# Kernel tuning notes

Hardware: AMD Instinct MI355X
Metric: run time of the kernel (lower is better)

Reference implementation:

```python
import jax, jax.numpy as jnp
import numpy as np
from jax import lax

WS = 7          # window_size
SHIFT = 0       # shift_size
HEADS = 6
EPS = 1e-12     # torch F.normalize default eps


def _window_partition(x, ws):
    B, C, H, W = x.shape
    x = x.reshape(B, C, H // ws, ws, W // ws, ws)
    # (B, H/ws, W/ws, C, ws, ws) -> (B*nW, C, ws, ws)
    return x.transpose(0, 2, 4, 1, 3, 5).reshape(-1, C, ws, ws)


def _window_reverse(win, B, C, H, W, ws):
    x = win.reshape(B, H // ws, W // ws, C, ws, ws)
    return x.transpose(0, 3, 1, 4, 2, 5).reshape(B, C, H, W)


def setup_inputs() -> dict:
    key = jax.random.key(0)
    ks = jax.random.split(key, 7)
    C = 192
    inp = {
        "x": jax.random.normal(ks[0], (4, C, 224, 224), jnp.float32),
        "w_qkv": jax.random.normal(ks[1], (3 * C, C), jnp.float32) * 0.02,
        "b_qkv": jax.random.normal(ks[2], (3 * C,), jnp.float32) * 0.02,
        "w_dw": jax.random.normal(ks[3], (3 * C, 1, 3, 3), jnp.float32) * 0.02,
        "b_dw": jax.random.normal(ks[4], (3 * C,), jnp.float32) * 0.02,
        "w_proj": jax.random.normal(ks[5], (C, C), jnp.float32) * 0.02,
        "b_proj": jax.random.normal(ks[6], (C,), jnp.float32) * 0.02,
        "temperature": jnp.ones((HEADS, 1, 1), jnp.float32),
    }
    return inp


def reference(x, w_qkv, b_qkv, w_dw, b_dw, w_proj, b_proj, temperature):
    B, C, H, W = x.shape
    pad_h = (WS - H % WS) % WS
    pad_w = (WS - W % WS) % WS
    if pad_h or pad_w:
        x = jnp.pad(x, ((0, 0), (0, 0), (0, pad_h), (0, pad_w)))
    Hp, Wp = H + pad_h, W + pad_w
    if SHIFT > 0:
        x = jnp.roll(x, shift=(-SHIFT, -SHIFT), axis=(2, 3))

    xw = _window_partition(x, WS)                     # (nW, C, ws, ws)

    # 1x1 conv qkv
    qkv = jnp.einsum('bchw,oc->bohw', xw, w_qkv) + b_qkv[None, :, None, None]
    # depthwise 3x3 conv, padding=1, groups=3C
    qkv = lax.conv_general_dilated(
        qkv, w_dw, window_strides=(1, 1), padding=((1, 1), (1, 1)),
        feature_group_count=3 * C,
        dimension_numbers=('NCHW', 'OIHW', 'NCHW')) + b_dw[None, :, None, None]

    q, k, v = jnp.split(qkv, 3, axis=1)               # each (nW, C, ws, ws)
    nW = q.shape[0]
    c = C // HEADS
    hw = WS * WS

    def heads(t):
        return t.reshape(nW, HEADS, c, hw)            # (nW, h, c, hw)

    q, k, v = heads(q), heads(k), heads(v)
    q = q / jnp.maximum(jnp.linalg.norm(q, axis=-2, keepdims=True), EPS)
    k = k / jnp.maximum(jnp.linalg.norm(k, axis=-2, keepdims=True), EPS)

    # attn[b,h,n,m] = sum_c k[b,h,c,n] * q[b,h,c,m], scaled by per-head temperature
    attn = jnp.einsum('bhcn,bhcm->bhnm', k, q) * temperature[None]
    attn = jax.nn.softmax(attn, axis=-2)
    out = jnp.einsum('bhcn,bhnm->bhcm', v, attn)      # (nW, h, c, hw)

    out = out.reshape(nW, C, WS, WS)
    out = _window_reverse(out, B, C, Hp, Wp, WS)
    out = jnp.einsum('bchw,oc->bohw', out, w_proj) + b_proj[None, :, None, None]

    if SHIFT > 0:
        out = jnp.roll(out, shift=(SHIFT, SHIFT), axis=(2, 3))
    if pad_h or pad_w:
        out = out[:, :, :H, :W]
    return out
```

## Files before the change

### kernel.cpp

```cpp
#include <hip/hip_runtime.h>
#include <math.h>

namespace {
constexpr int WSZ   = 7;
constexpr int HW    = 49;
constexpr int CIN   = 192;
constexpr int HEADS = 6;
constexpr int CH    = 32;
constexpr int IMG   = 224;
constexpr int ASTR  = 54;

__global__ __launch_bounds__(512, 4)
void win_attn_fused(const float* __restrict__ x,
                    const float* __restrict__ w_qkv,
                    const float* __restrict__ b_qkv,
                    const float* __restrict__ w_dw,
                    const float* __restrict__ b_dw,
                    const float* __restrict__ w_proj,
                    const float* __restrict__ b_proj,
                    const float* __restrict__ temperature,
                    float* __restrict__ out)
{
    __shared__ float xs[CIN][HW];
    __shared__ float qh[96][HW];
    __shared__ float attnb[HW][ASTR];
    __shared__ float outb[CH][HW];

    const int tid  = threadIdx.x;
    const int lane = tid & 63;
    const int wv   = __builtin_amdgcn_readfirstlane(tid >> 6);

    const int wi   = blockIdx.x;
    const int b    = wi >> 10;
    const int hy   = (wi >> 5) & 31;
    const int wx   = wi & 31;
    const int row0 = hy * WSZ, col0 = wx * WSZ;

    const int  p   = lane;
    const bool act = (lane < HW);
    const int  py  = p / WSZ, px = p % WSZ;

    for (int i = tid; i < CIN * HW; i += 512) {
        int c = i / HW, pp = i - c * HW;
        int gy = row0 + pp / WSZ, gx = col0 + pp % WSZ;
        xs[c][pp] = x[((b * CIN + c) * IMG + gy) * IMG + gx];
    }
    __syncthreads();

    float pacc[24];
    #pragma unroll
    for (int j = 0; j < 24; ++j) pacc[j] = 0.f;

    for (int h = 0; h < HEADS; ++h) {
        int oj[12];
        #pragma unroll
        for (int j = 0; j < 12; ++j) {
            int r = 12 * wv + j;
            oj[j] = (r < 32) ? (CH * h + r)
                  : (r < 64) ? (CIN + CH * h + (r - 32))
                             : (2 * CIN + CH * h + (r - 64));
        }

        if (act) {
            float acc[12];
            #pragma unroll
            for (int j = 0; j < 12; ++j) acc[j] = 0.f;
            #pragma unroll 4
            for (int c = 0; c < CIN; ++c) {
                float xv = xs[c][p];
                #pragma unroll
                for (int j = 0; j < 12; ++j)
                    acc[j] = fmaf(w_qkv[oj[j] * CIN + c], xv, acc[j]);
            }
            #pragma unroll
            for (int j = 0; j < 12; ++j)
                qh[12 * wv + j][p] = acc[j] + b_qkv[oj[j]];
        }

        if (act) {
            float cv[12];
            #pragma unroll
            for (int j = 0; j < 12; ++j) {
                int r = 12 * wv + j, o = oj[j];
                float s = b_dw[o];
                #pragma unroll
                for (int ky = 0; ky < 3; ++ky) {
                    int yy = py + ky - 1;
                    #pragma unroll
                    for (int kx = 0; kx < 3; ++kx) {
                        int xx = px + kx - 1;
                        bool ok = (yy >= 0) & (yy < WSZ) & (xx >= 0) & (xx < WSZ);
                        float v = ok ? qh[r][yy * WSZ + xx] : 0.f;
                        s = fmaf(w_dw[o * 9 + ky * 3 + kx], v, s);
                    }
                }
                cv[j] = s;
            }
            #pragma unroll
            for (int j = 0; j < 12; ++j) qh[12 * wv + j][p] = cv[j];
        }
        __syncthreads();

        float rnq = 0.f, rnk = 0.f;
        if (act) {
            float sq = 0.f, sk = 0.f;
            #pragma unroll
            for (int cc = 0; cc < CH; ++cc) {
                float a  = qh[cc][p];      sq = fmaf(a, a, sq);
                float bb = qh[CH + cc][p]; sk = fmaf(bb, bb, sk);
            }
            rnq = 1.0f / fmaxf(sqrtf(sq), 1e-12f);
            rnk = 1.0f / fmaxf(sqrtf(sk), 1e-12f);
        }

        float qreg[CH];
        if (act) {
            #pragma unroll
            for (int cc = 0; cc < CH; ++cc) qreg[cc] = qh[cc][p];
        }

        const float tmp = temperature[h];
        {
            int n0 = (wv * HW) >> 3;
            int n1 = ((wv + 1) * HW) >> 3;
            for (int n = n0; n < n1; ++n) {
                float rkn = __shfl(rnk, n);
                if (act) {
                    float s = 0.f;
                    #pragma unroll
                    for (int cc = 0; cc < CH; ++cc)
                        s = fmaf(qh[CH + cc][n], qreg[cc], s);
                    attnb[n][p] = s * tmp * rkn * rnq;
                }
            }
        }
        __syncthreads();

        {
            int m = tid >> 3, sub = tid & 7;
            if (m < HW) {
                int na = (sub * HW) >> 3;
                int nb = ((sub + 1) * HW) >> 3;
                float mx = -1e30f;
                for (int n = na; n < nb; ++n) mx = fmaxf(mx, attnb[n][m]);
                mx = fmaxf(mx, __shfl_xor(mx, 1));
                mx = fmaxf(mx, __shfl_xor(mx, 2));
                mx = fmaxf(mx, __shfl_xor(mx, 4));
                float sum = 0.f;
                for (int n = na; n < nb; ++n) {
                    float e = __expf(attnb[n][m] - mx);
                    attnb[n][m] = e;
                    sum += e;
                }
                sum += __shfl_xor(sum, 1);
                sum += __shfl_xor(sum, 2);
                sum += __shfl_xor(sum, 4);
                float inv = 1.0f / sum;
                for (int n = na; n < nb; ++n) attnb[n][m] *= inv;
            }
        }
        __syncthreads();

        if (act) {
            float s[4];
            #pragma unroll
            for (int j = 0; j < 4; ++j) s[j] = 0.f;
            for (int n = 0; n < HW; ++n) {
                float a = attnb[n][p];
                #pragma unroll
                for (int j = 0; j < 4; ++j)
                    s[j] = fmaf(qh[2 * CH + 4 * wv + j][n], a, s[j]);
            }
            #pragma unroll
            for (int j = 0; j < 4; ++j) outb[4 * wv + j][p] = s[j];
        }
        __syncthreads();

        if (act) {
            #pragma unroll 4
            for (int cc = 0; cc < CH; ++cc) {
                float ov = outb[cc][p];
                #pragma unroll
                for (int j = 0; j < 24; ++j)
                    pacc[j] = fmaf(w_proj[(24 * wv + j) * CIN + CH * h + cc], ov, pacc[j]);
            }
        }
    }

    if (act) {
        #pragma unroll
        for (int j = 0; j < 24; ++j) {
            int oc = 24 * wv + j;
            out[((b * CIN + oc) * IMG + row0 + py) * IMG + col0 + px] = pacc[j] + b_proj[oc];
        }
    }
}
}

extern "C" void kernel_launch(void* const* d_in, const int* in_sizes, int n_in,
                              void* d_out, int out_size, void* d_ws, size_t ws_size,
                              hipStream_t stream) {
    const float* x      = (const float*)d_in[0];
    const float* w_qkv  = (const float*)d_in[1];
    const float* b_qkv  = (const float*)d_in[2];
    const float* w_dw   = (const float*)d_in[3];
    const float* b_dw   = (const float*)d_in[4];
    const float* w_proj = (const float*)d_in[5];
    const float* b_proj = (const float*)d_in[6];
    const float* temp   = (const float*)d_in[7];

    win_attn_fused<<<dim3(4096), dim3(512), 0, stream>>>(
        x, w_qkv, b_qkv, w_dw, b_dw, w_proj, b_proj, temp, (float*)d_out);
}
```

Measured before the change: 4.515 ms.

## Stage windows through workspace with pre/post transpose kernels and float4 LDS reads

Adds a pre-pass kernel that copies image rows through shared memory into a contiguous per-window layout in the workspace, and a post-pass that scatters window outputs back to NCHW. The main kernel now reads each window as one contiguous chunk and stores it in LDS transposed (pixel-major, padded stride) so the QKV projection can use float4 LDS loads. The aim is to replace the strided 7-element global reads and writes of the fused kernel with coalesced traffic, at the price of an extra round trip of the full tensor through global memory and two more launches. A fallback to the original direct kernel runs when the workspace is too small.

```diff
diff --git a/kernel.cpp b/kernel.cpp
--- a/kernel.cpp
+++ b/kernel.cpp
@@ -9,19 +9,64 @@
 constexpr int CH    = 32;
 constexpr int IMG   = 224;
 constexpr int ASTR  = 54;
+constexpr int XSTR  = 196;
+constexpr int NWX   = 32;
+constexpr int CHUNK = CIN * HW;
+constexpr int NWIN  = 4 * 32 * 32;
+
+__global__ void win_pre(const float* __restrict__ x, float* __restrict__ win)
+{
+    __shared__ float tile[8][WSZ][IMG];
+    const int blk = blockIdx.x;
+    const int cg  = blk % 24;
+    const int hy  = (blk / 24) % 32;
+    const int b   = blk / (24 * 32);
+    const int c0  = cg * 8, row0 = hy * WSZ;
+
+    for (int i = threadIdx.x; i < 8 * WSZ * IMG; i += 256) {
+        int gx = i % IMG, ry = (i / IMG) % WSZ, c = i / (IMG * WSZ);
+        tile[c][ry][gx] = x[(((size_t)(b * CIN + c0 + c)) * IMG + row0 + ry) * IMG + gx];
+    }
+    __syncthreads();
+    for (int i = threadIdx.x; i < NWX * 8 * HW; i += 256) {
+        int p = i % HW, c = (i / HW) % 8, wx = i / (HW * 8);
+        size_t wi = ((size_t)(b * 32 + hy)) * NWX + wx;
+        win[wi * CHUNK + (c0 + c) * HW + p] = tile[c][p / WSZ][wx * WSZ + p % WSZ];
+    }
+}
+
+__global__ void win_post(const float* __restrict__ win, float* __restrict__ out)
+{
+    __shared__ float tile[8][WSZ][IMG];
+    const int blk = blockIdx.x;
+    const int cg  = blk % 24;
+    const int hy  = (blk / 24) % 32;
+    const int b   = blk / (24 * 32);
+    const int c0  = cg * 8, row0 = hy * WSZ;
+
+    for (int i = threadIdx.x; i < NWX * 8 * HW; i += 256) {
+        int p = i % HW, c = (i / HW) % 8, wx = i / (HW * 8);
+        size_t wi = ((size_t)(b * 32 + hy)) * NWX + wx;
+        tile[c][p / WSZ][wx * WSZ + p % WSZ] = win[wi * CHUNK + (c0 + c) * HW + p];
+    }
+    __syncthreads();
+    for (int i = threadIdx.x; i < 8 * WSZ * IMG; i += 256) {
+        int gx = i % IMG, ry = (i / IMG) % WSZ, c = i / (IMG * WSZ);
+        out[(((size_t)(b * CIN + c0 + c)) * IMG + row0 + ry) * IMG + gx] = tile[c][ry][gx];
+    }
+}
 
 __global__ __launch_bounds__(512, 4)
-void win_attn_fused(const float* __restrict__ x,
+void win_attn_fused(float* __restrict__ win,
                     const float* __restrict__ w_qkv,
                     const float* __restrict__ b_qkv,
                     const float* __restrict__ w_dw,
                     const float* __restrict__ b_dw,
                     const float* __restrict__ w_proj,
                     const float* __restrict__ b_proj,
-                    const float* __restrict__ temperature,
-                    float* __restrict__ out)
+                    const float* __restrict__ temperature)
 {
-    __shared__ float xs[CIN][HW];
+    __shared__ __align__(16) float xs[HW][XSTR];
     __shared__ float qh[96][HW];
     __shared__ float attnb[HW][ASTR];
     __shared__ float outb[CH][HW];
@@ -31,19 +76,14 @@
     const int wv   = __builtin_amdgcn_readfirstlane(tid >> 6);
 
     const int wi   = blockIdx.x;
-    const int b    = wi >> 10;
-    const int hy   = (wi >> 5) & 31;
-    const int wx   = wi & 31;
-    const int row0 = hy * WSZ, col0 = wx * WSZ;
-
     const int  p   = lane;
     const bool act = (lane < HW);
     const int  py  = p / WSZ, px = p % WSZ;
 
-    for (int i = tid; i < CIN * HW; i += 512) {
+    const float* __restrict__ xchunk = win + (size_t)wi * CHUNK;
+    for (int i = tid; i < CHUNK; i += 512) {
         int c = i / HW, pp = i - c * HW;
-        int gy = row0 + pp / WSZ, gx = col0 + pp % WSZ;
-        xs[c][pp] = x[((b * CIN + c) * IMG + gy) * IMG + gx];
+        xs[pp][c] = xchunk[i];
     }
     __syncthreads();
 
@@ -65,12 +105,20 @@
             float acc[12];
             #pragma unroll
             for (int j = 0; j < 12; ++j) acc[j] = 0.f;
-            #pragma unroll 4
-            for (int c = 0; c < CIN; ++c) {
-                float xv = xs[c][p];
-                #pragma unroll
-                for (int j = 0; j < 12; ++j)
-                    acc[j] = fmaf(w_qkv[oj[j] * CIN + c], xv, acc[j]);
+            const float4* xrow = (const float4*)(&xs[p][0]);
+            #pragma unroll 2
+            for (int c4 = 0; c4 < CIN / 4; ++c4) {
+                float4 xv = xrow[c4];
+                #pragma unroll
+                for (int j = 0; j < 12; ++j) {
+                    const float* wr = &w_qkv[oj[j] * CIN + 4 * c4];
+                    float a = acc[j];
+                    a = fmaf(wr[0], xv.x, a);
+                    a = fmaf(wr[1], xv.y, a);
+                    a = fmaf(wr[2], xv.z, a);
+                    a = fmaf(wr[3], xv.w, a);
+                    acc[j] = a;
+                }
             }
             #pragma unroll
             for (int j = 0; j < 12; ++j)
@@ -187,6 +235,193 @@
         }
     }
 
+    float* __restrict__ ochunk = win + (size_t)wi * CHUNK;
+    if (act) {
+        #pragma unroll
+        for (int j = 0; j < 24; ++j) {
+            int oc = 24 * wv + j;
+            ochunk[oc * HW + p] = pacc[j] + b_proj[oc];
+        }
+    }
+}
+
+__global__ __launch_bounds__(512, 4)
+void win_attn_direct(const float* __restrict__ x,
+                     const float* __restrict__ w_qkv,
+                     const float* __restrict__ b_qkv,
+                     const float* __restrict__ w_dw,
+                     const float* __restrict__ b_dw,
+                     const float* __restrict__ w_proj,
+                     const float* __restrict__ b_proj,
+                     const float* __restrict__ temperature,
+                     float* __restrict__ out)
+{
+    __shared__ float xs[CIN][HW];
+    __shared__ float qh[96][HW];
+    __shared__ float attnb[HW][ASTR];
+    __shared__ float outb[CH][HW];
+
+    const int tid  = threadIdx.x;
+    const int lane = tid & 63;
+    const int wv   = __builtin_amdgcn_readfirstlane(tid >> 6);
+
+    const int wi   = blockIdx.x;
+    const int b    = wi >> 10;
+    const int hy   = (wi >> 5) & 31;
+    const int wx   = wi & 31;
+    const int row0 = hy * WSZ, col0 = wx * WSZ;
+
+    const int  p   = lane;
+    const bool act = (lane < HW);
+    const int  py  = p / WSZ, px = p % WSZ;
+
+    for (int i = tid; i < CIN * HW; i += 512) {
+        int c = i / HW, pp = i - c * HW;
+        int gy = row0 + pp / WSZ, gx = col0 + pp % WSZ;
+        xs[c][pp] = x[((b * CIN + c) * IMG + gy) * IMG + gx];
+    }
+    __syncthreads();
+
+    float pacc[24];
+    #pragma unroll
+    for (int j = 0; j < 24; ++j) pacc[j] = 0.f;
+
+    for (int h = 0; h < HEADS; ++h) {
+        int oj[12];
+        #pragma unroll
+        for (int j = 0; j < 12; ++j) {
+            int r = 12 * wv + j;
+            oj[j] = (r < 32) ? (CH * h + r)
+                  : (r < 64) ? (CIN + CH * h + (r - 32))
+                             : (2 * CIN + CH * h + (r - 64));
+        }
+
+        if (act) {
+            float acc[12];
+            #pragma unroll
+            for (int j = 0; j < 12; ++j) acc[j] = 0.f;
+            #pragma unroll 4
+            for (int c = 0; c < CIN; ++c) {
+                float xv = xs[c][p];
+                #pragma unroll
+                for (int j = 0; j < 12; ++j)
+                    acc[j] = fmaf(w_qkv[oj[j] * CIN + c], xv, acc[j]);
+            }
+            #pragma unroll
+            for (int j = 0; j < 12; ++j)
+                qh[12 * wv + j][p] = acc[j] + b_qkv[oj[j]];
+        }
+
+        if (act) {
+            float cv[12];
+            #pragma unroll
+            for (int j = 0; j < 12; ++j) {
+                int r = 12 * wv + j, o = oj[j];
+                float s = b_dw[o];
+                #pragma unroll
+                for (int ky = 0; ky < 3; ++ky) {
+                    int yy = py + ky - 1;
+                    #pragma unroll
+                    for (int kx = 0; kx < 3; ++kx) {
+                        int xx = px + kx - 1;
+                        bool ok = (yy >= 0) & (yy < WSZ) & (xx >= 0) & (xx < WSZ);
+                        float v = ok ? qh[r][yy * WSZ + xx] : 0.f;
+                        s = fmaf(w_dw[o * 9 + ky * 3 + kx], v, s);
+                    }
+                }
+                cv[j] = s;
+            }
+            #pragma unroll
+            for (int j = 0; j < 12; ++j) qh[12 * wv + j][p] = cv[j];
+        }
+        __syncthreads();
+
+        float rnq = 0.f, rnk = 0.f;
+        if (act) {
+            float sq = 0.f, sk = 0.f;
+            #pragma unroll
+            for (int cc = 0; cc < CH; ++cc) {
+                float a  = qh[cc][p];      sq = fmaf(a, a, sq);
+                float bb = qh[CH + cc][p]; sk = fmaf(bb, bb, sk);
+            }
+            rnq = 1.0f / fmaxf(sqrtf(sq), 1e-12f);
+            rnk = 1.0f / fmaxf(sqrtf(sk), 1e-12f);
+        }
+
+        float qreg[CH];
+        if (act) {
+            #pragma unroll
+            for (int cc = 0; cc < CH; ++cc) qreg[cc] = qh[cc][p];
+        }
+
+        const float tmp = temperature[h];
+        {
+            int n0 = (wv * HW) >> 3;
+            int n1 = ((wv + 1) * HW) >> 3;
+            for (int n = n0; n < n1; ++n) {
+                float rkn = __shfl(rnk, n);
+                if (act) {
+                    float s = 0.f;
+                    #pragma unroll
+                    for (int cc = 0; cc < CH; ++cc)
+                        s = fmaf(qh[CH + cc][n], qreg[cc], s);
+                    attnb[n][p] = s * tmp * rkn * rnq;
+                }
+            }
+        }
+        __syncthreads();
+
+        {
+            int m = tid >> 3, sub = tid & 7;
+            if (m < HW) {
+                int na = (sub * HW) >> 3;
+                int nb = ((sub + 1) * HW) >> 3;
+                float mx = -1e30f;
+                for (int n = na; n < nb; ++n) mx = fmaxf(mx, attnb[n][m]);
+                mx = fmaxf(mx, __shfl_xor(mx, 1));
+                mx = fmaxf(mx, __shfl_xor(mx, 2));
+                mx = fmaxf(mx, __shfl_xor(mx, 4));
+                float sum = 0.f;
+                for (int n = na; n < nb; ++n) {
+                    float e = __expf(attnb[n][m] - mx);
+                    attnb[n][m] = e;
+                    sum += e;
+                }
+                sum += __shfl_xor(sum, 1);
+                sum += __shfl_xor(sum, 2);
+                sum += __shfl_xor(sum, 4);
+                float inv = 1.0f / sum;
+                for (int n = na; n < nb; ++n) attnb[n][m] *= inv;
+            }
+        }
+        __syncthreads();
+
+        if (act) {
+            float s[4];
+            #pragma unroll
+            for (int j = 0; j < 4; ++j) s[j] = 0.f;
+            for (int n = 0; n < HW; ++n) {
+                float a = attnb[n][p];
+                #pragma unroll
+                for (int j = 0; j < 4; ++j)
+                    s[j] = fmaf(qh[2 * CH + 4 * wv + j][n], a, s[j]);
+            }
+            #pragma unroll
+            for (int j = 0; j < 4; ++j) outb[4 * wv + j][p] = s[j];
+        }
+        __syncthreads();
+
+        if (act) {
+            #pragma unroll 4
+            for (int cc = 0; cc < CH; ++cc) {
+                float ov = outb[cc][p];
+                #pragma unroll
+                for (int j = 0; j < 24; ++j)
+                    pacc[j] = fmaf(w_proj[(24 * wv + j) * CIN + CH * h + cc], ov, pacc[j]);
+            }
+        }
+    }
+
     if (act) {
         #pragma unroll
         for (int j = 0; j < 24; ++j) {
@@ -209,6 +444,16 @@
     const float* b_proj = (const float*)d_in[6];
     const float* temp   = (const float*)d_in[7];
 
-    win_attn_fused<<<dim3(4096), dim3(512), 0, stream>>>(
-        x, w_qkv, b_qkv, w_dw, b_dw, w_proj, b_proj, temp, (float*)d_out);
-}
+    const size_t WS_NEEDED = (size_t)NWIN * CHUNK * sizeof(float);
+
+    if (d_ws != nullptr && ws_size >= WS_NEEDED) {
+        float* ws = (float*)d_ws;
+        win_pre<<<dim3(4 * 32 * 24), dim3(256), 0, stream>>>(x, ws);
+        win_attn_fused<<<dim3(NWIN), dim3(512), 0, stream>>>(
+            ws, w_qkv, b_qkv, w_dw, b_dw, w_proj, b_proj, temp);
+        win_post<<<dim3(4 * 32 * 24), dim3(256), 0, stream>>>(ws, (float*)d_out);
+    } else {
+        win_attn_direct<<<dim3(NWIN), dim3(512), 0, stream>>>(
+            x, w_qkv, b_qkv, w_dw, b_dw, w_proj, b_proj, temp, (float*)d_out);
+    }
+}
```

After: 3.888 ms. -13.9%, faster.
